# Optimization experiments

Hardware: AMD Instinct MI355X
Metric: run time of the kernel (lower is better)

The kernel has to match this reference:

```python
import jax, jax.numpy as jnp
import numpy as np


def setup_inputs() -> dict:
    key = jax.random.key(0)
    kx, kd = jax.random.split(key)
    B, S, D = 32, 1024, 512
    x = jax.random.normal(kx, (B, S, D), dtype=jnp.float32)
    # per-token repeat counts in [1, 9): mean ~4.5 frames per phoneme
    durations = jax.random.randint(kd, (B, S), 1, 9, dtype=jnp.int32)
    return {"x": x, "durations": durations}


def reference(x, durations):
    """Duration-based token expansion (FastSpeech LengthRegulator).

    Replaces the per-token repeat/cat/pad Python loops with a single
    vectorized gather driven by cumulative duration offsets.
    Returns (expanded_x, mel_len, mel_mask) matching the torch module's
    (expanded_x, target=None, mel_len, mel_mask) with target omitted
    (projection is None in this configuration).
    """
    B, S, D = x.shape
    csum = jnp.cumsum(durations, axis=1)          # [B,S] end offset of each token
    mel_len = csum[:, -1]                         # [B]
    # max_len is data-dependent, same as the torch module's max over batch.
    max_len = int(jax.device_get(jnp.max(mel_len)))
    t = jnp.arange(max_len)                       # [T]
    # output frame t belongs to token j iff csum[j-1] <= t < csum[j]
    idx = jax.vmap(lambda c: jnp.searchsorted(c, t, side="right"))(csum)  # [B,T]
    idx = jnp.minimum(idx, S - 1)                 # clamp padding region
    expanded = jnp.take_along_axis(x, idx[:, :, None], axis=1)  # [B,T,D]
    mel_mask = t[None, :] >= mel_len[:, None]     # [B,T] True where padded
    expanded = jnp.where(mel_mask[:, :, None], jnp.zeros((), x.dtype), expanded)
    return expanded, mel_len, mel_mask
```

## Files before the change

kernel.cpp:

```cpp
#include <hip/hip_runtime.h>
#include <hip/hip_bf16.h>


#define S_TOK 1024
#define B_SZ  32

__global__ __launch_bounds__(S_TOK)
void lr_cumsum_kernel(const int* __restrict__ dur,
                      int* __restrict__ csum,
                      float* __restrict__ mel_len_out) {
    const int b = blockIdx.x;
    const int tid = threadIdx.x;
    __shared__ int buf[S_TOK];
    buf[tid] = dur[b * S_TOK + tid];
    __syncthreads();
    for (int off = 1; off < S_TOK; off <<= 1) {
        int add = (tid >= off) ? buf[tid - off] : 0;
        __syncthreads();
        buf[tid] += add;
        __syncthreads();
    }
    csum[b * S_TOK + tid] = buf[tid];
    if (tid == S_TOK - 1) mel_len_out[b] = (float)buf[tid];
}

__global__ __launch_bounds__(128)
void lr_expand_kernel(const float* __restrict__ x,
                      const int* __restrict__ csum,
                      float* __restrict__ out,
                      float* __restrict__ mask,
                      int D, int max_len) {
    const int t = blockIdx.x;
    const int b = blockIdx.y;
    const int tid = threadIdx.x;
    const int* __restrict__ c = csum + b * S_TOK;
    const int mel = c[S_TOK - 1];

    float4* __restrict__ orow =
        (float4*)(out + ((size_t)b * max_len + t) * (size_t)D);

    if (t >= mel) {
        orow[tid] = make_float4(0.f, 0.f, 0.f, 0.f);
        if (tid == 0) mask[(size_t)b * max_len + t] = 1.0f;
        return;
    }

    int lo = 0, hi = S_TOK;
    while (lo < hi) {
        int mid = (lo + hi) >> 1;
        if (c[mid] > t) hi = mid; else lo = mid + 1;
    }
    const int idx = lo;

    const float4* __restrict__ xrow =
        (const float4*)(x + ((size_t)b * S_TOK + idx) * (size_t)D);
    orow[tid] = xrow[tid];
    if (tid == 0) mask[(size_t)b * max_len + t] = 0.0f;
}

extern "C" void kernel_launch(void* const* d_in, const int* in_sizes, int n_in,
                              void* d_out, int out_size, void* d_ws, size_t ws_size,
                              hipStream_t stream) {
    const float* x = (const float*)d_in[0];
    const int* dur = (const int*)d_in[1];
    float* out = (float*)d_out;

    const int D = in_sizes[0] / in_sizes[1];
    const int max_len = (out_size / B_SZ - 1) / (D + 1);

    int* csum = (int*)d_ws;
    float* mel_len = out + (size_t)B_SZ * max_len * D;
    float* mask = mel_len + B_SZ;

    lr_cumsum_kernel<<<B_SZ, S_TOK, 0, stream>>>(dur, csum, mel_len);

    dim3 grid((unsigned)max_len, (unsigned)B_SZ);
    lr_expand_kernel<<<grid, 128, 0, stream>>>(x, csum, out, mask, D, max_len);
}
```

Baseline: 416.1 us.

## Replace per-frame gather with per-token scatter and separate tail/mask kernels

Launches one block per input token, which loads the token row once and writes it to all its repeated output frames. This removes the per-frame binary search and repeated reads of x. Zero-padding of frames past mel_len and the mask are written by two separate kernels. In exchange there are extra kernel launches, tail blocks that mostly exit immediately, and uneven per-block write counts.

Result: faster. 370.8 us (-10.9%).

```diff
diff --git a/kernel.cpp b/kernel.cpp
--- a/kernel.cpp
+++ b/kernel.cpp
@@ -25,37 +25,54 @@
 }
 
 __global__ __launch_bounds__(128)
-void lr_expand_kernel(const float* __restrict__ x,
-                      const int* __restrict__ csum,
-                      float* __restrict__ out,
-                      float* __restrict__ mask,
-                      int D, int max_len) {
-    const int t = blockIdx.x;
+void lr_scatter_kernel(const float* __restrict__ x,
+                       const int* __restrict__ csum,
+                       float* __restrict__ out,
+                       int D, int max_len) {
+    const int s = blockIdx.x;
     const int b = blockIdx.y;
     const int tid = threadIdx.x;
     const int* __restrict__ c = csum + b * S_TOK;
-    const int mel = c[S_TOK - 1];
+    const int base = (s == 0) ? 0 : c[s - 1];
+    const int end  = c[s];
 
-    float4* __restrict__ orow =
-        (float4*)(out + ((size_t)b * max_len + t) * (size_t)D);
+    const float4 v =
+        ((const float4*)(x + ((size_t)b * S_TOK + s) * (size_t)D))[tid];
+    float4* __restrict__ o =
+        (float4*)(out + ((size_t)b * max_len + base) * (size_t)D) + tid;
+    const int d4 = D >> 2;
+    for (int r = 0; r < end - base; ++r) {
+        o[(size_t)r * d4] = v;
+    }
+}
 
-    if (t >= mel) {
-        orow[tid] = make_float4(0.f, 0.f, 0.f, 0.f);
-        if (tid == 0) mask[(size_t)b * max_len + t] = 1.0f;
-        return;
+__global__ __launch_bounds__(128)
+void lr_tail_kernel(const int* __restrict__ csum,
+                    float* __restrict__ out,
+                    int D, int max_len) {
+    const int b = blockIdx.y;
+    const int tid = threadIdx.x;
+    const int mel = csum[b * S_TOK + S_TOK - 1];
+    const int t0 = mel + blockIdx.x * 4;
+    if (t0 >= max_len) return;
+    const float4 z = make_float4(0.f, 0.f, 0.f, 0.f);
+#pragma unroll
+    for (int k = 0; k < 4; ++k) {
+        const int t = t0 + k;
+        if (t < max_len)
+            ((float4*)(out + ((size_t)b * max_len + t) * (size_t)D))[tid] = z;
     }
+}
 
-    int lo = 0, hi = S_TOK;
-    while (lo < hi) {
-        int mid = (lo + hi) >> 1;
-        if (c[mid] > t) hi = mid; else lo = mid + 1;
-    }
-    const int idx = lo;
-
-    const float4* __restrict__ xrow =
-        (const float4*)(x + ((size_t)b * S_TOK + idx) * (size_t)D);
-    orow[tid] = xrow[tid];
-    if (tid == 0) mask[(size_t)b * max_len + t] = 0.0f;
+__global__ __launch_bounds__(256)
+void lr_mask_kernel(const int* __restrict__ csum,
+                    float* __restrict__ mask,
+                    int max_len) {
+    const int b = blockIdx.y;
+    const int t = blockIdx.x * 256 + threadIdx.x;
+    if (t >= max_len) return;
+    const int mel = csum[b * S_TOK + S_TOK - 1];
+    mask[(size_t)b * max_len + t] = (t >= mel) ? 1.0f : 0.0f;
 }
 
 extern "C" void kernel_launch(void* const* d_in, const int* in_sizes, int n_in,
@@ -74,6 +91,12 @@
 
     lr_cumsum_kernel<<<B_SZ, S_TOK, 0, stream>>>(dur, csum, mel_len);
 
-    dim3 grid((unsigned)max_len, (unsigned)B_SZ);
-    lr_expand_kernel<<<grid, 128, 0, stream>>>(x, csum, out, mask, D, max_len);
+    dim3 sgrid((unsigned)S_TOK, (unsigned)B_SZ);
+    lr_scatter_kernel<<<sgrid, D / 4, 0, stream>>>(x, csum, out, D, max_len);
+
+    dim3 tgrid((unsigned)((max_len + 3) / 4), (unsigned)B_SZ);
+    lr_tail_kernel<<<tgrid, D / 4, 0, stream>>>(csum, out, D, max_len);
+
+    dim3 mgrid((unsigned)((max_len + 255) / 256), (unsigned)B_SZ);
+    lr_mask_kernel<<<mgrid, 256, 0, stream>>>(csum, mask, max_len);
 }
```

## Scatter token rows by duration instead of per-frame binary-search gather

Applied to the files above, without the earlier changes.

The expand kernel now launches one block per input token. Each block reads its row of x once and writes it `dur` times using nontemporal stores. Separate tail blocks zero the padded frames and fill the mask, which removes the per-output-frame binary search over the cumsum. The 1024-thread shared-memory cumsum is replaced by a single-wave kernel: each lane scans 16 values sequentially, then the lane totals are combined with a shuffle scan. This cuts the block count and redundant searches, but gives uneven per-block work (1–8 rows per token).

Result: faster. 353.1 us (-15.1%).

```diff
diff --git a/kernel.cpp b/kernel.cpp
--- a/kernel.cpp
+++ b/kernel.cpp
@@ -5,57 +5,82 @@
 #define S_TOK 1024
 #define B_SZ  32
 
-__global__ __launch_bounds__(S_TOK)
-void lr_cumsum_kernel(const int* __restrict__ dur,
-                      int* __restrict__ csum,
-                      float* __restrict__ mel_len_out) {
+typedef float vfloat4 __attribute__((ext_vector_type(4)));
+
+__global__ __launch_bounds__(64)
+void lr_scan_kernel(const int* __restrict__ dur,
+                    int* __restrict__ csum,
+                    float* __restrict__ mel_len_out) {
     const int b = blockIdx.x;
-    const int tid = threadIdx.x;
-    __shared__ int buf[S_TOK];
-    buf[tid] = dur[b * S_TOK + tid];
-    __syncthreads();
-    for (int off = 1; off < S_TOK; off <<= 1) {
-        int add = (tid >= off) ? buf[tid - off] : 0;
-        __syncthreads();
-        buf[tid] += add;
-        __syncthreads();
+    const int lane = threadIdx.x;
+    const int* __restrict__ d = dur + b * S_TOK;
+
+    int v[16];
+    int sum = 0;
+#pragma unroll
+    for (int k = 0; k < 16; ++k) {
+        v[k] = d[lane * 16 + k];
+        sum += v[k];
     }
-    csum[b * S_TOK + tid] = buf[tid];
-    if (tid == S_TOK - 1) mel_len_out[b] = (float)buf[tid];
+    int run = 0;
+#pragma unroll
+    for (int k = 0; k < 16; ++k) { run += v[k]; v[k] = run; }
+
+    int tot = sum;
+#pragma unroll
+    for (int off = 1; off < 64; off <<= 1) {
+        int n = __shfl_up(tot, off, 64);
+        if (lane >= off) tot += n;
+    }
+    const int excl = tot - sum;
+
+#pragma unroll
+    for (int k = 0; k < 16; ++k)
+        csum[b * S_TOK + lane * 16 + k] = v[k] + excl;
+    if (lane == 63) mel_len_out[b] = (float)tot;
 }
 
 __global__ __launch_bounds__(128)
-void lr_expand_kernel(const float* __restrict__ x,
-                      const int* __restrict__ csum,
-                      float* __restrict__ out,
-                      float* __restrict__ mask,
-                      int D, int max_len) {
-    const int t = blockIdx.x;
+void lr_fused_kernel(const float* __restrict__ x,
+                     const int* __restrict__ csum,
+                     float* __restrict__ out,
+                     float* __restrict__ mask,
+                     int D, int max_len) {
     const int b = blockIdx.y;
     const int tid = threadIdx.x;
     const int* __restrict__ c = csum + b * S_TOK;
-    const int mel = c[S_TOK - 1];
+    const int d4 = D >> 2;
 
-    float4* __restrict__ orow =
-        (float4*)(out + ((size_t)b * max_len + t) * (size_t)D);
+    if (blockIdx.x < S_TOK) {
+        const int s = blockIdx.x;
+        const int base = (s == 0) ? 0 : c[s - 1];
+        const int dur = c[s] - base;
 
-    if (t >= mel) {
-        orow[tid] = make_float4(0.f, 0.f, 0.f, 0.f);
-        if (tid == 0) mask[(size_t)b * max_len + t] = 1.0f;
-        return;
+        const vfloat4 v =
+            ((const vfloat4*)(x + ((size_t)b * S_TOK + s) * (size_t)D))[tid];
+        vfloat4* __restrict__ o =
+            (vfloat4*)(out + ((size_t)b * max_len + base) * (size_t)D) + tid;
+        for (int r = 0; r < dur; ++r)
+            __builtin_nontemporal_store(v, o + (size_t)r * d4);
+        if (tid < dur)
+            mask[(size_t)b * max_len + base + tid] = 0.0f;
+    } else {
+        const int mel = c[S_TOK - 1];
+        const int t0 = mel + (blockIdx.x - S_TOK) * 4;
+        if (t0 >= max_len) return;
+        const vfloat4 z = (vfloat4)(0.f);
+#pragma unroll
+        for (int k = 0; k < 4; ++k) {
+            const int t = t0 + k;
+            if (t < max_len) {
+                vfloat4* __restrict__ o =
+                    (vfloat4*)(out + ((size_t)b * max_len + t) * (size_t)D) + tid;
+                __builtin_nontemporal_store(z, o);
+            }
+        }
+        if (tid < 4 && t0 + tid < max_len)
+            mask[(size_t)b * max_len + t0 + tid] = 1.0f;
     }
-
-    int lo = 0, hi = S_TOK;
-    while (lo < hi) {
-        int mid = (lo + hi) >> 1;
-        if (c[mid] > t) hi = mid; else lo = mid + 1;
-    }
-    const int idx = lo;
-
-    const float4* __restrict__ xrow =
-        (const float4*)(x + ((size_t)b * S_TOK + idx) * (size_t)D);
-    orow[tid] = xrow[tid];
-    if (tid == 0) mask[(size_t)b * max_len + t] = 0.0f;
 }
 
 extern "C" void kernel_launch(void* const* d_in, const int* in_sizes, int n_in,
@@ -72,8 +97,9 @@
     float* mel_len = out + (size_t)B_SZ * max_len * D;
     float* mask = mel_len + B_SZ;
 
-    lr_cumsum_kernel<<<B_SZ, S_TOK, 0, stream>>>(dur, csum, mel_len);
+    lr_scan_kernel<<<B_SZ, 64, 0, stream>>>(dur, csum, mel_len);
 
-    dim3 grid((unsigned)max_len, (unsigned)B_SZ);
-    lr_expand_kernel<<<grid, 128, 0, stream>>>(x, csum, out, mask, D, max_len);
+    const int tail_blocks = (max_len > S_TOK) ? ((max_len - S_TOK + 3) / 4 + 1) : 1;
+    dim3 fgrid((unsigned)(S_TOK + tail_blocks), (unsigned)B_SZ);
+    lr_fused_kernel<<<fgrid, 128, 0, stream>>>(x, csum, out, mask, D, max_len);
 }
```
